# Optimization experiments

Measured on AMD Instinct MI355X. Metric: run time of the kernel, lower is better.

The kernel has to match this reference:

```python
import jax, jax.numpy as jnp
import numpy as np

N_OBJS = 100          # max detections / scatter buffer size
TOP_K = 100           # top_k_n peaks per channel
KP_THRES = 0.3        # score threshold before NMS
NMS_IOU = 0.5
RESIZE_H, RESIZE_W = 1536.0, 1536.0   # resize_shape (== heatmap HxW here)
H, W = 1536, 1536


def _peak_hms(hms):
    # 3x3 stride-1 SAME max pool; keep only local maxima (Base.apply_max_pool)
    hmax = jax.lax.reduce_window(hms, -jnp.inf, jax.lax.max, (1, 3, 3, 1), (1, 1, 1, 1), 'SAME')
    return jnp.where(hms == hmax, hms, 0.0)


def _top_k_loc(hms, k):
    # per-channel top-k peak coordinates -> [b, c, k, 2] (y, x) int32
    b, h, w, c = hms.shape
    flat = jnp.transpose(hms, (0, 3, 1, 2)).reshape(b, c, h * w)
    _, idx = jax.lax.top_k(flat, k)
    return jnp.stack([idx // w, idx % w], axis=-1).astype(jnp.int32)


def _iou_matrix(boxes):
    # boxes [N,4] = (y1,x1,y2,x2)
    y1, x1, y2, x2 = boxes[:, 0], boxes[:, 1], boxes[:, 2], boxes[:, 3]
    area = jnp.maximum(y2 - y1, 0.0) * jnp.maximum(x2 - x1, 0.0)
    iy1 = jnp.maximum(y1[:, None], y1[None, :]); ix1 = jnp.maximum(x1[:, None], x1[None, :])
    iy2 = jnp.minimum(y2[:, None], y2[None, :]); ix2 = jnp.minimum(x2[:, None], x2[None, :])
    inter = jnp.maximum(iy2 - iy1, 0.0) * jnp.maximum(ix2 - ix1, 0.0)
    union = area[:, None] + area[None, :] - inter
    return inter / jnp.maximum(union, 1e-8)


def _nms_single(boxes, scores):
    # greedy single-class NMS, fixed-size (combined_non_max_suppression equivalent,
    # clip_boxes=False, score_threshold=-inf); padded slots are zeros like TF.
    order = jnp.argsort(-scores)
    boxes, scores = boxes[order], scores[order]
    n = boxes.shape[0]
    iou = _iou_matrix(boxes)
    idxs = jnp.arange(n)

    def step(suppressed, inp):
        i, iou_row = inp
        keep_i = ~suppressed[i]
        return suppressed | (keep_i & (iou_row > NMS_IOU) & (idxs > i)), keep_i

    _, keep = jax.lax.scan(step, jnp.zeros(n, bool), (idxs, iou))
    perm = jnp.argsort(jnp.where(keep, 0, 1))  # stable: compact kept to front, score order preserved
    keep_s = keep[perm]
    out_boxes = jnp.where(keep_s[:, None], boxes[perm], 0.0)
    out_scores = jnp.where(keep_s, scores[perm], 0.0)
    return out_boxes, out_scores, jnp.zeros(n, jnp.float32)


def _forward(obj_heat_map, offset_map, size_maps, origin_shapes):
    resize_shape = jnp.array([RESIZE_H, RESIZE_W], jnp.float32)
    ratio = origin_shapes / resize_shape                      # [b,2]
    hms = _peak_hms(obj_heat_map)                             # [b,H,W,2]
    b = hms.shape[0]
    coors = _top_k_loc(hms, TOP_K)                            # [b,2,K,2]
    b_coors, b_lnmks = coors[:, :1], coors[:, 1:]             # obj / nose coords
    bidx = jnp.arange(b)[:, None, None]

    # nose landmark: scores at nose-channel peaks, masked mean of coords (int mean like TF)
    nose_scores = hms[bidx, b_lnmks[..., 0], b_lnmks[..., 1], 1]     # [b,1,K]
    nose_mask = nose_scores > 0.5
    cnt = jnp.maximum(jnp.sum(nose_mask), 1)
    lnmk_mean = jnp.sum(jnp.where(nose_mask[..., None], b_lnmks, 0), axis=(0, 1, 2)) // cnt
    b_lnmks_m = lnmk_mean.reshape(b, 1, 2)                    # requires b == 1 (as in original)
    b_nose_scores = jnp.where(nose_mask, nose_scores, -1.0).reshape(b, -1)

    # boxes from sizes at object peaks
    size_vals = size_maps[bidx, b_coors[..., 0], b_coors[..., 1]]    # [b,1,K,2]
    obj_scores = hms[bidx, b_coors[..., 0], b_coors[..., 1], 0]      # [b,1,K]
    centers = b_coors.astype(jnp.float32)
    tls = jnp.maximum(centers - size_vals / 2.0, 0.0)
    brs = jnp.minimum(centers + size_vals / 2.0, resize_shape - 1.0)
    bboxes = jnp.concatenate([tls, brs], axis=-1) * jnp.tile(ratio, (1, 2))[:, None, None, :]
    bboxes, scores = bboxes[:, 0], obj_scores[:, 0]           # [b,K,4], [b,K]

    # scatter masked candidates into -1-initialized buffer (tensor_scatter_nd_update equivalent)
    mask = scores > KP_THRES
    cand = jnp.where(mask[..., None], jnp.concatenate([bboxes, scores[..., None]], -1), -1.0)
    cand = jnp.pad(cand, ((0, 0), (0, N_OBJS - TOP_K), (0, 0)), constant_values=-1.0)  # [b,N_OBJS,5]

    nb, ns, nc = jax.vmap(_nms_single)(cand[..., :4], cand[..., 4])
    box_results = jnp.where(nb == -1.0, jnp.inf, nb)
    box_results = jnp.where(box_results == 0.0, jnp.inf, box_results)  # (x - 1 == -1)
    b_bboxes = jnp.concatenate([box_results, ns[..., None], nc[..., None]], axis=-1)  # [b,N_OBJS,6]

    # offset vectors at the mean nose landmark (gather 8ch -> [b,n,4,2])
    bidx2 = jnp.arange(b)[:, None]
    off = offset_map[bidx2, b_lnmks_m[..., 0], b_lnmks_m[..., 1]].reshape(b, 1, 4, 2)
    lf = b_lnmks_m.astype(jnp.float32)
    b_ENM = (lf[:, :, None, :] - off) * ratio[:, None, None, :]
    b_lnmks_out = lf * ratio[:, None, :]
    return b_bboxes, b_lnmks_out, b_ENM, b_nose_scores


def setup_inputs() -> dict:
    key = jax.random.key(0)
    k1, k2, k3 = jax.random.split(key, 3)
    obj_heat_map = jax.random.uniform(k1, (1, H, W, 2), jnp.float32)
    offset_map = jax.random.normal(k2, (1, H, W, 8), jnp.float32) * 8.0
    size_maps = jax.random.uniform(k3, (1, H, W, 2), jnp.float32) * 128.0
    origin_shapes = jnp.array([[1080.0, 1920.0]], jnp.float32)
    return {"obj_heat_map": obj_heat_map, "offset_map": offset_map,
            "size_maps": size_maps, "origin_shapes": origin_shapes}


def reference(obj_heat_map, offset_map, size_maps, origin_shapes):
    return _forward(obj_heat_map, offset_map, size_maps, origin_shapes)
```

## Files before the change

### kernel.cpp

```cpp
#include <hip/hip_runtime.h>
#include <cstdint>

#define IW 1536
#define IH 1536
#define TOPK 100
#define CAPP 327680
#define CAPB 128
#define CAPT 8192
#define BF_INF16 0x7F7Fu

typedef unsigned u32; typedef unsigned long long u64; typedef unsigned short u16;

#define OH1   0
#define OCNT  4096
#define OSEL  4102
#define OLSD  4106
#define OZEND 4172
#define OPK   4172
#define OPV   (OPK + 2*CAPP)
#define OLB   (OPV + CAPP)
#define OLT   (OLB + 4*CAPB)

__device__ __forceinline__ u32 enc16(u32 b){ b &= 0xFFFFu; return (b & 0x8000u) ? ((~b)&0xFFFFu) : (b|0x8000u); }
__device__ __forceinline__ u32 dec16(u32 e){ return (e & 0x8000u) ? (e^0x8000u) : ((~e)&0xFFFFu); }
__device__ __forceinline__ float up16(u32 b){ return __uint_as_float((b&0xFFFFu)<<16); }
__device__ __forceinline__ u16 f2bf(float f){ u32 u=__float_as_uint(f); return (u16)((u + 0x7FFFu + ((u>>16)&1u))>>16); }

__device__ __forceinline__ void wave_sel2048(const u32* bins, u32 need, int* Dout, u32* Aout){
  int lane = threadIdx.x & 63;
  u32 s = 0;
  #pragma unroll
  for(int k=0;k<32;++k) s += bins[lane*32+k];
  u32 c = s;
  #pragma unroll
  for(int off=1;off<64;off<<=1){
    u32 v = __shfl_down(c, off, 64);
    if(lane + off < 64) c += v;
  }
  u32 cnext = __shfl_down(c, 1, 64); if(lane==63) cnext = 0u;
  u64 m = __ballot(c >= need);
  if(m == 0ull){ if(lane==0){ *Dout = 0; *Aout = 0u; } return; }
  int L = 63 - __builtin_clzll((unsigned long long)m);
  if(lane == L){
    u32 above = cnext; int D = 32*L;
    for(int b=32*L+31; b>=32*L; --b){
      u32 h = bins[b];
      if(above + h >= need){ D = b; break; }
      above += h;
    }
    *Dout = D; *Aout = above;
  }
}

__global__ __launch_bounds__(1024) void scan_kernel(const u32* __restrict__ hm, u32* __restrict__ ws){
  __shared__ u32 lh[4096];
  __shared__ u32 lbuf[2][1600];
  __shared__ u16 vbuf[2][1600];
  __shared__ u32 lcnt[2], lbase[2];
  int tid = threadIdx.x, lane = tid & 63;
  for(int i=tid;i<4096;i+=1024) lh[i]=0u;
  if(tid<2) lcnt[tid]=0u;
  __syncthreads();

  int p = (blockIdx.x*1024 + tid)*4;
  int y = p / IW, x = p - y*IW;
  const u32* R1 = hm + y*IW;
  const u32* R0 = y ? R1 - IW : R1;
  const u32* R2 = (y < IH-1) ? R1 + IW : R1;
  uint4 c0 = *(const uint4*)(R0+x), c1 = *(const uint4*)(R1+x), c2 = *(const uint4*)(R2+x);
  int xl = x ? x-1 : 0, xr = (x+4 < IW) ? x+4 : IW-1;
  u32 a0[6] = {R0[xl], c0.x, c0.y, c0.z, c0.w, R0[xr]};
  u32 a1[6] = {R1[xl], c1.x, c1.y, c1.z, c1.w, R1[xr]};
  u32 a2[6] = {R2[xl], c2.x, c2.y, c2.z, c2.w, R2[xr]};

  #pragma unroll
  for(int j=0;j<4;++j){
    u32 cc = a1[j+1];
    u32 cl = cc & 0xFFFFu, chv = cc >> 16;
    u32 m0=0u, m1=0u;
    #pragma unroll
    for(int d=0;d<3;++d){
      u32 n0=a0[j+d], n2=a2[j+d]; u32 t;
      t=n0&0xFFFFu; m0=t>m0?t:m0;  t=n0>>16; m1=t>m1?t:m1;
      t=n2&0xFFFFu; m0=t>m0?t:m0;  t=n2>>16; m1=t>m1?t:m1;
    }
    { u32 n=a1[j];   u32 t=n&0xFFFFu; m0=t>m0?t:m0; t=n>>16; m1=t>m1?t:m1; }
    { u32 n=a1[j+2]; u32 t=n&0xFFFFu; m0=t>m0?t:m0; t=n>>16; m1=t>m1?t:m1; }
    bool pk0 = (cl >= m0), pk1 = (chv >= m1);
    u32 idx = (u32)(p + j);

    u64 mk0 = __ballot(pk0);
    if(mk0){
      u32 cw = __popcll(mk0), b;
      if(lane==0) b = atomicAdd(&lcnt[0], cw);
      b = __shfl(b, 0);
      if(pk0){
        u32 pos = b + __popcll(mk0 & ((1ull<<lane)-1ull));
        if(pos < 1600){ lbuf[0][pos] = idx; vbuf[0][pos] = (u16)cl; }
      }
    }
    u64 mk1 = __ballot(pk1);
    if(mk1){
      u32 cw = __popcll(mk1), b;
      if(lane==0) b = atomicAdd(&lcnt[1], cw);
      b = __shfl(b, 0);
      if(pk1){
        u32 pos = b + __popcll(mk1 & ((1ull<<lane)-1ull));
        if(pos < 1600){ lbuf[1][pos] = idx; vbuf[1][pos] = (u16)chv; }
      }
    }
    if(pk0) atomicAdd(&lh[enc16(cl)>>5], 1u);
    if(pk1) atomicAdd(&lh[2048 + (enc16(chv)>>5)], 1u);
  }
  __syncthreads();
  if(tid < 2){
    u32 n = lcnt[tid]; if(n > 1600) n = 1600;
    lcnt[tid] = n;
    lbase[tid] = atomicAdd(&ws[OCNT+tid], n);
  }
  __syncthreads();
  u16* pv = (u16*)(ws + OPV);
  for(int ch=0;ch<2;++ch){
    u32 n = lcnt[ch], base = lbase[ch];
    for(u32 i=tid;i<n;i+=1024){
      u32 g = base + i;
      if(g < CAPP){ ws[OPK + ch*CAPP + g] = lbuf[ch][i]; pv[ch*CAPP + g] = vbuf[ch][i]; }
    }
  }
  for(int i=tid;i<4096;i+=1024) if(lh[i]) atomicAdd(&ws[OH1+i], lh[i]);
}

#define GRID2 128
__global__ __launch_bounds__(1024) void mid_kernel(u32* __restrict__ ws){
  __shared__ u32 lhh[4096];
  __shared__ u64 tbuf[2][2048];
  __shared__ u32 tcnt[2], tbase[2];
  __shared__ u32 lsdl[64];
  __shared__ int Dsh[2]; __shared__ u32 Ash[2];
  int tid = threadIdx.x, lane = tid & 63;
  for(int i=tid;i<4096;i+=1024) lhh[i] = ws[OH1+i];
  if(tid < 2) tcnt[tid] = 0u;
  if(tid < 64) lsdl[tid] = 0u;
  __syncthreads();
  if(tid < 64)       wave_sel2048(lhh,        (u32)TOPK, &Dsh[0], &Ash[0]);
  else if(tid < 128) wave_sel2048(lhh + 2048, (u32)TOPK, &Dsh[1], &Ash[1]);
  __syncthreads();
  if(blockIdx.x == 0 && tid < 2){ ws[OSEL+tid] = (u32)Dsh[tid]; ws[OSEL+2+tid] = Ash[tid]; }

  const u16* pv = (const u16*)(ws + OPV);
  u64* listB = (u64*)(ws + OLB);
  for(int ch=0;ch<2;++ch){
    u32 n = ws[OCNT+ch]; if(n > CAPP) n = CAPP;
    int D = Dsh[ch];
    for(u32 base = blockIdx.x*1024; base < n; base += GRID2*1024){
      u32 i = base + tid;
      bool act = (i < n);
      u32 e = 0, idx = 0;
      if(act){ e = enc16(pv[ch*CAPP + i]); idx = ws[OPK + ch*CAPP + i]; }
      if(act && (int)(e>>5) > D){
        u32 pos = atomicAdd(&ws[OCNT+2+ch], 1u);
        if(pos < CAPB) listB[ch*CAPB + pos] = ((u64)e<<32) | (u32)(~idx);
      }
      bool isT = act && ((int)(e>>5) == D);
      if(isT) atomicAdd(&lsdl[ch*32 + (e & 31u)], 1u);
      u64 mk = __ballot(isT);
      if(mk){
        u32 cw = __popcll(mk), b;
        if(lane==0) b = atomicAdd(&tcnt[ch], cw);
        b = __shfl(b, 0);
        if(isT){
          u32 pos = b + __popcll(mk & ((1ull<<lane)-1ull));
          if(pos < 2048) tbuf[ch][pos] = ((u64)e<<32) | (u32)(~idx);
        }
      }
    }
  }
  __syncthreads();
  if(tid < 2){
    u32 c = tcnt[tid]; if(c > 2048) c = 2048;
    tcnt[tid] = c;
    tbase[tid] = atomicAdd(&ws[OCNT+4+tid], c);
  }
  __syncthreads();
  u64* tie = (u64*)(ws + OLT);
  for(int ch=0;ch<2;++ch)
    for(u32 i=tid;i<tcnt[ch];i+=1024){
      u32 g = tbase[ch] + i;
      if(g < CAPT) tie[ch*CAPT + g] = tbuf[ch][i];
    }
  if(tid < 64 && lsdl[tid]) atomicAdd(&ws[OLSD + tid], lsdl[tid]);
}

__global__ __launch_bounds__(512) void finalize_kernel(
    u32* __restrict__ ws, const u32* __restrict__ szm, const u16* __restrict__ offm,
    const u16* __restrict__ orig, u16* __restrict__ out){
  __shared__ u32 tidxS[2][CAPT];
  __shared__ u32 h2s[2][2048];
  __shared__ u64 keysS[2][CAPB];
  __shared__ u32 selS[2][CAPB];
  __shared__ u32 wbitsS[2][64];
  __shared__ u32 lsdS[64];
  __shared__ u32 hdr[10];
  __shared__ int selcS[2], selc2S[2], BvS[2], LshS[2], tcS[2];
  __shared__ float oval[TOPK]; __shared__ int oidx[TOPK];
  __shared__ float nval[TOPK]; __shared__ int nidx[TOPK];
  __shared__ float cbox[TOPK][4]; __shared__ float cscore[TOPK]; __shared__ float area[TOPK];
  __shared__ int sup[TOPK]; __shared__ int slotv[TOPK];
  __shared__ u64 nbits[2*TOPK];
  __shared__ u64 suppS[2];
  __shared__ int cS, srS, scS, meanr, meanc;
  int tid = threadIdx.x, lane = tid & 63;
  int ch = tid >> 8, ltid = tid & 255;

  if(tid < 10) hdr[tid] = ws[OCNT + tid];
  if(tid < 64) lsdS[tid] = ws[OLSD + tid];
  for(int i=tid;i<4096;i+=512) ((u32*)h2s)[i] = 0u;
  if(tid < 128) ((u32*)wbitsS)[tid] = 0u;
  if(tid < 4){ selcS[tid&1] = 0; selc2S[tid&1] = 0; }
  if(tid < 2){ BvS[tid] = 0; LshS[tid] = 0; tcS[tid] = 0; }
  if(tid < TOPK){ oval[tid]=0.0f; oidx[tid]=0; nval[tid]=0.0f; nidx[tid]=0; }
  __syncthreads();

  int nB = (int)hdr[2+ch]; if(nB > CAPB) nB = CAPB;
  int nT = (int)hdr[4+ch]; if(nT > CAPT) nT = CAPT;
  int D  = (int)hdr[6+ch];
  u32 above = hdr[8+ch];
  const u64* listB = ((const u64*)(ws + OLB)) + ch*CAPB;
  const u64* tie   = ((const u64*)(ws + OLT)) + ch*CAPT;
  float* dval = ch ? nval : oval;
  int*   didx = ch ? nidx : oidx;

  if(ltid < 64){
    u32 h = (lane < 32) ? lsdS[ch*32 + lane] : 0u;
    u32 c = h;
    #pragma unroll
    for(int off=1;off<32;off<<=1){
      u32 v = __shfl_down(c, off, 64);
      if(lane + off < 32) c += v;
    }
    u32 need2 = (u32)TOPK - above;
    u64 m = __ballot(lane >= 1 && lane < 32 && c >= need2);
    if(lane == 0){
      LshS[ch] = m ? (63 - __builtin_clzll((unsigned long long)m)) : 0;
      selcS[ch] = nB;
    }
  }
  for(int i=ltid;i<nB;i+=256) keysS[ch][i] = listB[i];
  __syncthreads();
  u32 thr = ((u32)D<<5) | (u32)LshS[ch];
  float tval = up16(dec16(thr));

  for(int base2=0; base2<nT; base2+=256){
    int i = base2 + ltid;
    bool act = (i < nT);
    u64 k = 0; u32 e = 0, idx = 0;
    if(act){ k = tie[i]; e = (u32)(k>>32); idx = ~(u32)(k & 0xFFFFFFFFu); }
    if(act && e > thr){
      int pos = atomicAdd(&selcS[ch], 1); if(pos < CAPB) keysS[ch][pos] = k;
    }
    bool isT = act && (e == thr);
    u64 mk = __ballot(isT);
    if(mk){
      u32 cw = __popcll(mk), b;
      if(lane==0) b = (u32)atomicAdd(&tcS[ch], (int)cw);
      b = __shfl(b, 0);
      if(isT){
        u32 pos = b + __popcll(mk & ((1ull<<lane)-1ull));
        if(pos < CAPT) tidxS[ch][pos] = idx;
      }
    }
    if(isT) atomicAdd(&h2s[ch][idx>>11], 1u);
  }
  __syncthreads();

  int nA = selcS[ch]; if(nA > CAPB) nA = CAPB; if(nA > TOPK) nA = TOPK;
  int need = TOPK - nA;
  if(ltid < nA){
    u64 kreg = keysS[ch][ltid];
    int r = 0;
    for(int j=0;j<nA;++j) r += (keysS[ch][j] > kreg);
    if(r < TOPK){
      dval[r] = up16(dec16((u32)(kreg>>32)));
      didx[r] = (int)(~(u32)(kreg & 0xFFFFFFFFu));
    }
  }
  if(ltid < 64){
    const u32* hh = h2s[ch];
    int base = lane*32;
    u32 s = 0;
    #pragma unroll
    for(int k2=0;k2<32;++k2) s += hh[base+k2];
    u32 c = s;
    #pragma unroll
    for(int off=1;off<64;off<<=1){
      u32 v = __shfl_up(c, off, 64);
      if(lane >= off) c += v;
    }
    u64 m = __ballot(need > 0 && c >= (u32)need);
    int L = m ? (int)(__ffsll((unsigned long long)m) - 1) : -1;
    if(L >= 0 && lane == L){
      u32 hb[32];
      #pragma unroll
      for(int k2=0;k2<32;++k2) hb[k2] = hh[base+k2];
      u32 cum2 = c - s;
      int Bsel = base;
      #pragma unroll
      for(int k2=0;k2<32;++k2){
        if(cum2 + hb[k2] >= (u32)need){ Bsel = base+k2; break; }
        cum2 += hb[k2];
      }
      BvS[ch] = Bsel;
    }
  }
  __syncthreads();

  int B = BvS[ch];
  int tc = tcS[ch]; if(tc > CAPT) tc = CAPT;
  if(need > 0){
    for(int i=ltid;i<tc;i+=256){
      u32 idx = tidxS[ch][i];
      int b = (int)(idx>>11);
      if(b < B){
        int pos = atomicAdd(&selc2S[ch], 1);
        if(pos < CAPB) selS[ch][pos] = idx;
      } else if(b == B){
        atomicOr(&wbitsS[ch][(idx&2047)>>5], 1u<<(idx&31));
      }
    }
  }
  __syncthreads();

  int sc = selc2S[ch]; if(sc > CAPB) sc = CAPB;
  if(need > 0 && ltid < sc){
    u32 v = selS[ch][ltid];
    int r = 0;
    for(int j=0;j<sc;++j) r += (selS[ch][j] < v);
    if(nA + r < TOPK){ dval[nA+r] = tval; didx[nA+r] = (int)v; }
  }
  if(need > 0 && ltid < 64){
    u32 bits = wbitsS[ch][ltid];
    u32 cnt = __popc(bits);
    u32 incl = cnt;
    #pragma unroll
    for(int off=1;off<64;off<<=1){
      u32 v = __shfl_up(incl, off, 64);
      if(lane >= off) incl += v;
    }
    int excl = (int)(incl - cnt);
    int rem = need - sc;
    int pos = nA + sc + excl;
    int j = 0;
    while(bits){
      int l = __ffs(bits) - 1; bits &= bits - 1;
      if(excl + j < rem && pos + j < TOPK){
        dval[pos+j] = tval;
        didx[pos+j] = (int)(((u32)B<<11) | ((u32)ltid<<5) | (u32)l);
      }
      ++j;
    }
  }
  __syncthreads();

  float ry = up16(orig[0]) / 1536.0f;
  float rx = up16(orig[1]) / 1536.0f;

  if(tid == 0){ cS = 0; srS = 0; scS = 0; }
  __syncthreads();
  if(tid < TOPK && nval[tid] > 0.5f){
    atomicAdd(&cS, 1);
    atomicAdd(&srS, nidx[tid] / IW);
    atomicAdd(&scS, nidx[tid] % IW);
  }
  if(tid < TOPK) out[610 + tid] = f2bf(nval[tid] > 0.5f ? nval[tid] : -1.0f);
  __syncthreads();
  if(tid == 0){
    int c = cS < 1 ? 1 : cS;
    meanr = srS / c; meanc = scS / c;
  }

  if(tid < TOPK){
    int idx = oidx[tid];
    int r = idx / IW, c = idx - r*IW;
    float score = oval[tid];
    u32 sz = szm[idx];
    float sy = up16(sz), sx = up16(sz>>16);
    float cy = (float)r, cx = (float)c;
    float tly = fmaxf(cy - sy*0.5f, 0.0f);
    float tlx = fmaxf(cx - sx*0.5f, 0.0f);
    float bry = fminf(cy + sy*0.5f, 1535.0f);
    float brx = fminf(cx + sx*0.5f, 1535.0f);
    bool mk = score > 0.3f;
    float b0 = mk ? tly*ry : -1.0f;
    float b1 = mk ? tlx*rx : -1.0f;
    float b2 = mk ? bry*ry : -1.0f;
    float b3 = mk ? brx*rx : -1.0f;
    cbox[tid][0]=b0; cbox[tid][1]=b1; cbox[tid][2]=b2; cbox[tid][3]=b3;
    cscore[tid] = mk ? score : -1.0f;
    area[tid] = fmaxf(b2-b0,0.0f) * fmaxf(b3-b1,0.0f);
  }
  if(tid < 2*TOPK) nbits[tid] = 0ull;
  __syncthreads();

  for(int t=tid; t<TOPK*TOPK; t+=512){
    int i = t / TOPK, j = t - i*TOPK;
    if(j > i){
      float iy1 = fmaxf(cbox[i][0], cbox[j][0]);
      float ix1 = fmaxf(cbox[i][1], cbox[j][1]);
      float iy2 = fminf(cbox[i][2], cbox[j][2]);
      float ix2 = fminf(cbox[i][3], cbox[j][3]);
      float inter = fmaxf(iy2-iy1,0.0f) * fmaxf(ix2-ix1,0.0f);
      float uni = (area[i] + area[j]) - inter;
      if(inter / fmaxf(uni, 1e-8f) > 0.5f)
        atomicOr(&nbits[i*2 + (j>>6)], 1ull << (j&63));
    }
  }
  __syncthreads();
  if(tid == 0){
    u64 s0 = 0ull, s1 = 0ull;
    for(int base=0;base<TOPK;base+=10){
      u64 buf[20];
      #pragma unroll
      for(int k=0;k<20;++k) buf[k] = nbits[2*base+k];
      #pragma unroll
      for(int k=0;k<10;++k){
        int i = base+k;
        bool su = (i<64) ? ((s0>>i)&1ull) : ((s1>>(i-64))&1ull);
        if(!su){ s0 |= buf[2*k]; s1 |= buf[2*k+1]; }
      }
    }
    suppS[0] = s0; suppS[1] = s1;
  }
  __syncthreads();
  if(tid < TOPK) sup[tid] = (int)((suppS[tid>>6] >> (tid&63)) & 1ull);
  __syncthreads();

  if(tid < TOPK){
    int kbefore = 0, sbefore = 0, ktot = 0;
    for(int j=0;j<TOPK;++j){
      int sj = sup[j];
      ktot += (1 - sj);
      if(j < tid){ kbefore += (1 - sj); sbefore += sj; }
    }
    int slot = sup[tid] ? (ktot + sbefore) : kbefore;
    slotv[slot] = tid;
  }
  __syncthreads();

  if(tid < TOPK){
    int s = slotv[tid];
    bool ks = !sup[s];
    u16 row[6];
    if(ks){
      for(int d=0;d<4;++d){
        float v = cbox[s][d];
        row[d] = (v == -1.0f || v == 0.0f) ? (u16)BF_INF16 : f2bf(v);
      }
      row[4] = f2bf(cscore[s]);
    } else {
      for(int d=0;d<4;++d) row[d] = (u16)BF_INF16;
      row[4] = 0;
    }
    row[5] = 0;
    for(int d=0;d<6;++d) out[tid*6 + d] = row[d];
  }

  if(tid == 0){
    float lfy = (float)meanr, lfx = (float)meanc;
    out[600] = f2bf(lfy * ry);
    out[601] = f2bf(lfx * rx);
    const u16* op = offm + ((size_t)meanr*IW + meanc)*8;
    for(int p=0;p<4;++p){
      out[602 + p*2 + 0] = f2bf((lfy - up16(op[p*2+0])) * ry);
      out[602 + p*2 + 1] = f2bf((lfx - up16(op[p*2+1])) * rx);
    }
  }
}

extern "C" void kernel_launch(void* const* d_in, const int* in_sizes, int n_in,
                              void* d_out, int out_size, void* d_ws, size_t ws_size,
                              hipStream_t stream) {
  const u32* heat = (const u32*)d_in[0];
  const u16* offm = (const u16*)d_in[1];
  const u32* szm  = (const u32*)d_in[2];
  const u16* orig = (const u16*)d_in[3];
  u16* out = (u16*)d_out;
  u32* ws = (u32*)d_ws;

  hipMemsetAsync(ws, 0, OZEND*sizeof(u32), stream);
  scan_kernel<<<576, 1024, 0, stream>>>(heat, ws);
  mid_kernel<<<GRID2, 1024, 0, stream>>>(ws);
  finalize_kernel<<<1, 512, 0, stream>>>(ws, szm, offm, orig, out);
}
```

Baseline: 183.2 us.

## Fuse scan, mid and finalize kernels into one persistent kernel with grid barriers

Result: slower. 197.3 us (+7.7%).

```diff
diff --git a/kernel.cpp b/kernel.cpp
--- a/kernel.cpp
+++ b/kernel.cpp
@@ -9,12 +9,16 @@
 #define CAPT 8192
 #define BF_INF16 0x7F7Fu
 
+#define NBLK 192
+#define VBTOT 576
+
 typedef unsigned u32; typedef unsigned long long u64; typedef unsigned short u16;
 
 #define OH1   0
 #define OCNT  4096
 #define OSEL  4102
 #define OLSD  4106
+#define OBAR  4170
 #define OZEND 4172
 #define OPK   4172
 #define OPV   (OPK + 2*CAPP)
@@ -52,125 +56,166 @@
   }
 }
 
-__global__ __launch_bounds__(1024) void scan_kernel(const u32* __restrict__ hm, u32* __restrict__ ws){
-  __shared__ u32 lh[4096];
-  __shared__ u32 lbuf[2][1600];
-  __shared__ u16 vbuf[2][1600];
-  __shared__ u32 lcnt[2], lbase[2];
+union SMem {
+  struct {
+    u32 lh[4096];
+    u32 lbuf[2][1600];
+    u16 vbuf[2][1600];
+  } a;
+  struct {
+    u32 lhh[4096];
+    u64 tbuf[2][2048];
+    u32 lsdl[64];
+  } b;
+  struct {
+    u32 tidxS[2][CAPT];
+    u32 h2s[2][2048];
+    u64 keysS[2][CAPB];
+    u32 selS[2][CAPB];
+    u32 wbitsS[2][64];
+    u32 lsdS[64];
+    u32 hdr[10];
+    float oval[TOPK]; int oidx[TOPK];
+    float nval[TOPK]; int nidx[TOPK];
+    float cbox[TOPK][4]; float cscore[TOPK]; float area[TOPK];
+    int sup[TOPK]; int slotv[TOPK];
+    u64 nbits[2*TOPK];
+  } c;
+};
+
+__global__ __launch_bounds__(1024, 4) void fused_kernel(
+    const u32* __restrict__ hm, u32* __restrict__ ws,
+    const u32* __restrict__ szm, const u16* __restrict__ offm,
+    const u16* __restrict__ orig, u16* __restrict__ out){
+  __shared__ SMem S;
+  __shared__ u32 lcnt[2], lbase[2], tcnt[2], tbase[2];
+  __shared__ int Dsh[2]; __shared__ u32 Ash[2];
+  __shared__ int selcS[2], selc2S[2], BvS[2], LshS[2], tcS[2];
+  __shared__ u64 suppS[2];
+  __shared__ int cS, srS, scS, meanr, meanc;
+
   int tid = threadIdx.x, lane = tid & 63;
-  for(int i=tid;i<4096;i+=1024) lh[i]=0u;
-  if(tid<2) lcnt[tid]=0u;
-  __syncthreads();
-
-  int p = (blockIdx.x*1024 + tid)*4;
-  int y = p / IW, x = p - y*IW;
-  const u32* R1 = hm + y*IW;
-  const u32* R0 = y ? R1 - IW : R1;
-  const u32* R2 = (y < IH-1) ? R1 + IW : R1;
-  uint4 c0 = *(const uint4*)(R0+x), c1 = *(const uint4*)(R1+x), c2 = *(const uint4*)(R2+x);
-  int xl = x ? x-1 : 0, xr = (x+4 < IW) ? x+4 : IW-1;
-  u32 a0[6] = {R0[xl], c0.x, c0.y, c0.z, c0.w, R0[xr]};
-  u32 a1[6] = {R1[xl], c1.x, c1.y, c1.z, c1.w, R1[xr]};
-  u32 a2[6] = {R2[xl], c2.x, c2.y, c2.z, c2.w, R2[xr]};
-
-  #pragma unroll
-  for(int j=0;j<4;++j){
-    u32 cc = a1[j+1];
-    u32 cl = cc & 0xFFFFu, chv = cc >> 16;
-    u32 m0=0u, m1=0u;
+
+  for(int i=tid;i<4096;i+=1024) S.a.lh[i]=0u;
+  for(int vb = blockIdx.x; vb < VBTOT; vb += NBLK){
+    __syncthreads();
+    if(tid<2) lcnt[tid]=0u;
+    __syncthreads();
+
+    int p = (vb*1024 + tid)*4;
+    int y = p / IW, x = p - y*IW;
+    const u32* R1 = hm + y*IW;
+    const u32* R0 = y ? R1 - IW : R1;
+    const u32* R2 = (y < IH-1) ? R1 + IW : R1;
+    uint4 c0 = *(const uint4*)(R0+x), c1 = *(const uint4*)(R1+x), c2 = *(const uint4*)(R2+x);
+    int xl = x ? x-1 : 0, xr = (x+4 < IW) ? x+4 : IW-1;
+    u32 a0[6] = {R0[xl], c0.x, c0.y, c0.z, c0.w, R0[xr]};
+    u32 a1[6] = {R1[xl], c1.x, c1.y, c1.z, c1.w, R1[xr]};
+    u32 a2[6] = {R2[xl], c2.x, c2.y, c2.z, c2.w, R2[xr]};
+
     #pragma unroll
-    for(int d=0;d<3;++d){
-      u32 n0=a0[j+d], n2=a2[j+d]; u32 t;
-      t=n0&0xFFFFu; m0=t>m0?t:m0;  t=n0>>16; m1=t>m1?t:m1;
-      t=n2&0xFFFFu; m0=t>m0?t:m0;  t=n2>>16; m1=t>m1?t:m1;
-    }
-    { u32 n=a1[j];   u32 t=n&0xFFFFu; m0=t>m0?t:m0; t=n>>16; m1=t>m1?t:m1; }
-    { u32 n=a1[j+2]; u32 t=n&0xFFFFu; m0=t>m0?t:m0; t=n>>16; m1=t>m1?t:m1; }
-    bool pk0 = (cl >= m0), pk1 = (chv >= m1);
-    u32 idx = (u32)(p + j);
-
-    u64 mk0 = __ballot(pk0);
-    if(mk0){
-      u32 cw = __popcll(mk0), b;
-      if(lane==0) b = atomicAdd(&lcnt[0], cw);
-      b = __shfl(b, 0);
-      if(pk0){
-        u32 pos = b + __popcll(mk0 & ((1ull<<lane)-1ull));
-        if(pos < 1600){ lbuf[0][pos] = idx; vbuf[0][pos] = (u16)cl; }
-      }
-    }
-    u64 mk1 = __ballot(pk1);
-    if(mk1){
-      u32 cw = __popcll(mk1), b;
-      if(lane==0) b = atomicAdd(&lcnt[1], cw);
-      b = __shfl(b, 0);
-      if(pk1){
-        u32 pos = b + __popcll(mk1 & ((1ull<<lane)-1ull));
-        if(pos < 1600){ lbuf[1][pos] = idx; vbuf[1][pos] = (u16)chv; }
-      }
-    }
-    if(pk0) atomicAdd(&lh[enc16(cl)>>5], 1u);
-    if(pk1) atomicAdd(&lh[2048 + (enc16(chv)>>5)], 1u);
-  }
-  __syncthreads();
-  if(tid < 2){
-    u32 n = lcnt[tid]; if(n > 1600) n = 1600;
-    lcnt[tid] = n;
-    lbase[tid] = atomicAdd(&ws[OCNT+tid], n);
-  }
-  __syncthreads();
-  u16* pv = (u16*)(ws + OPV);
-  for(int ch=0;ch<2;++ch){
-    u32 n = lcnt[ch], base = lbase[ch];
-    for(u32 i=tid;i<n;i+=1024){
-      u32 g = base + i;
-      if(g < CAPP){ ws[OPK + ch*CAPP + g] = lbuf[ch][i]; pv[ch*CAPP + g] = vbuf[ch][i]; }
-    }
-  }
-  for(int i=tid;i<4096;i+=1024) if(lh[i]) atomicAdd(&ws[OH1+i], lh[i]);
-}
-
-#define GRID2 128
-__global__ __launch_bounds__(1024) void mid_kernel(u32* __restrict__ ws){
-  __shared__ u32 lhh[4096];
-  __shared__ u64 tbuf[2][2048];
-  __shared__ u32 tcnt[2], tbase[2];
-  __shared__ u32 lsdl[64];
-  __shared__ int Dsh[2]; __shared__ u32 Ash[2];
-  int tid = threadIdx.x, lane = tid & 63;
-  for(int i=tid;i<4096;i+=1024) lhh[i] = ws[OH1+i];
+    for(int j=0;j<4;++j){
+      u32 cc = a1[j+1];
+      u32 cl = cc & 0xFFFFu, chv = cc >> 16;
+      u32 m0=0u, m1=0u;
+      #pragma unroll
+      for(int d=0;d<3;++d){
+        u32 n0=a0[j+d], n2=a2[j+d]; u32 t;
+        t=n0&0xFFFFu; m0=t>m0?t:m0;  t=n0>>16; m1=t>m1?t:m1;
+        t=n2&0xFFFFu; m0=t>m0?t:m0;  t=n2>>16; m1=t>m1?t:m1;
+      }
+      { u32 n=a1[j];   u32 t=n&0xFFFFu; m0=t>m0?t:m0; t=n>>16; m1=t>m1?t:m1; }
+      { u32 n=a1[j+2]; u32 t=n&0xFFFFu; m0=t>m0?t:m0; t=n>>16; m1=t>m1?t:m1; }
+      bool pk0 = (cl >= m0), pk1 = (chv >= m1);
+      u32 idx = (u32)(p + j);
+
+      u64 mk0 = __ballot(pk0);
+      if(mk0){
+        u32 cw = __popcll(mk0), b;
+        if(lane==0) b = atomicAdd(&lcnt[0], cw);
+        b = __shfl(b, 0);
+        if(pk0){
+          u32 pos = b + __popcll(mk0 & ((1ull<<lane)-1ull));
+          if(pos < 1600){ S.a.lbuf[0][pos] = idx; S.a.vbuf[0][pos] = (u16)cl; }
+        }
+      }
+      u64 mk1 = __ballot(pk1);
+      if(mk1){
+        u32 cw = __popcll(mk1), b;
+        if(lane==0) b = atomicAdd(&lcnt[1], cw);
+        b = __shfl(b, 0);
+        if(pk1){
+          u32 pos = b + __popcll(mk1 & ((1ull<<lane)-1ull));
+          if(pos < 1600){ S.a.lbuf[1][pos] = idx; S.a.vbuf[1][pos] = (u16)chv; }
+        }
+      }
+      if(pk0) atomicAdd(&S.a.lh[enc16(cl)>>5], 1u);
+      if(pk1) atomicAdd(&S.a.lh[2048 + (enc16(chv)>>5)], 1u);
+    }
+    __syncthreads();
+    if(tid < 2){
+      u32 n = lcnt[tid]; if(n > 1600) n = 1600;
+      lcnt[tid] = n;
+      lbase[tid] = atomicAdd(&ws[OCNT+tid], n);
+    }
+    __syncthreads();
+    {
+      u16* pvw = (u16*)(ws + OPV);
+      for(int ch2=0;ch2<2;++ch2){
+        u32 n = lcnt[ch2], base = lbase[ch2];
+        for(u32 i=tid;i<n;i+=1024){
+          u32 g = base + i;
+          if(g < CAPP){ ws[OPK + ch2*CAPP + g] = S.a.lbuf[ch2][i]; pvw[ch2*CAPP + g] = S.a.vbuf[ch2][i]; }
+        }
+      }
+    }
+  }
+  __syncthreads();
+  for(int i=tid;i<4096;i+=1024) if(S.a.lh[i]) atomicAdd(&ws[OH1+i], S.a.lh[i]);
+
+  __syncthreads();
+  if(tid==0){
+    __hip_atomic_fetch_add(&ws[OBAR], 1u, __ATOMIC_RELEASE, __HIP_MEMORY_SCOPE_AGENT);
+    while(__hip_atomic_load(&ws[OBAR], __ATOMIC_ACQUIRE, __HIP_MEMORY_SCOPE_AGENT) < (u32)NBLK)
+      __builtin_amdgcn_s_sleep(2);
+  }
+  __syncthreads();
+
+  for(int i=tid;i<4096;i+=1024) S.b.lhh[i] = ws[OH1+i];
   if(tid < 2) tcnt[tid] = 0u;
-  if(tid < 64) lsdl[tid] = 0u;
-  __syncthreads();
-  if(tid < 64)       wave_sel2048(lhh,        (u32)TOPK, &Dsh[0], &Ash[0]);
-  else if(tid < 128) wave_sel2048(lhh + 2048, (u32)TOPK, &Dsh[1], &Ash[1]);
+  if(tid < 64) S.b.lsdl[tid] = 0u;
+  __syncthreads();
+  if(tid < 64)       wave_sel2048(S.b.lhh,        (u32)TOPK, &Dsh[0], &Ash[0]);
+  else if(tid < 128) wave_sel2048(S.b.lhh + 2048, (u32)TOPK, &Dsh[1], &Ash[1]);
   __syncthreads();
   if(blockIdx.x == 0 && tid < 2){ ws[OSEL+tid] = (u32)Dsh[tid]; ws[OSEL+2+tid] = Ash[tid]; }
 
-  const u16* pv = (const u16*)(ws + OPV);
-  u64* listB = (u64*)(ws + OLB);
-  for(int ch=0;ch<2;++ch){
-    u32 n = ws[OCNT+ch]; if(n > CAPP) n = CAPP;
-    int D = Dsh[ch];
-    for(u32 base = blockIdx.x*1024; base < n; base += GRID2*1024){
-      u32 i = base + tid;
-      bool act = (i < n);
-      u32 e = 0, idx = 0;
-      if(act){ e = enc16(pv[ch*CAPP + i]); idx = ws[OPK + ch*CAPP + i]; }
-      if(act && (int)(e>>5) > D){
-        u32 pos = atomicAdd(&ws[OCNT+2+ch], 1u);
-        if(pos < CAPB) listB[ch*CAPB + pos] = ((u64)e<<32) | (u32)(~idx);
-      }
-      bool isT = act && ((int)(e>>5) == D);
-      if(isT) atomicAdd(&lsdl[ch*32 + (e & 31u)], 1u);
-      u64 mk = __ballot(isT);
-      if(mk){
-        u32 cw = __popcll(mk), b;
-        if(lane==0) b = atomicAdd(&tcnt[ch], cw);
-        b = __shfl(b, 0);
-        if(isT){
-          u32 pos = b + __popcll(mk & ((1ull<<lane)-1ull));
-          if(pos < 2048) tbuf[ch][pos] = ((u64)e<<32) | (u32)(~idx);
+  {
+    const u16* pvr = (const u16*)(ws + OPV);
+    u64* listBw = (u64*)(ws + OLB);
+    for(int ch2=0;ch2<2;++ch2){
+      u32 n = ws[OCNT+ch2]; if(n > CAPP) n = CAPP;
+      int D2 = Dsh[ch2];
+      for(u32 base = blockIdx.x*1024; base < n; base += (u32)NBLK*1024){
+        u32 i = base + tid;
+        bool act = (i < n);
+        u32 e = 0, idx = 0;
+        if(act){ e = enc16(pvr[ch2*CAPP + i]); idx = ws[OPK + ch2*CAPP + i]; }
+        if(act && (int)(e>>5) > D2){
+          u32 pos = atomicAdd(&ws[OCNT+2+ch2], 1u);
+          if(pos < CAPB) listBw[ch2*CAPB + pos] = ((u64)e<<32) | (u32)(~idx);
+        }
+        bool isT = act && ((int)(e>>5) == D2);
+        if(isT) atomicAdd(&S.b.lsdl[ch2*32 + (e & 31u)], 1u);
+        u64 mk = __ballot(isT);
+        if(mk){
+          u32 cw = __popcll(mk), b;
+          if(lane==0) b = atomicAdd(&tcnt[ch2], cw);
+          b = __shfl(b, 0);
+          if(isT){
+            u32 pos = b + __popcll(mk & ((1ull<<lane)-1ull));
+            if(pos < 2048) S.b.tbuf[ch2][pos] = ((u64)e<<32) | (u32)(~idx);
+          }
         }
       }
     }
@@ -182,296 +227,306 @@
     tbase[tid] = atomicAdd(&ws[OCNT+4+tid], c);
   }
   __syncthreads();
-  u64* tie = (u64*)(ws + OLT);
-  for(int ch=0;ch<2;++ch)
-    for(u32 i=tid;i<tcnt[ch];i+=1024){
-      u32 g = tbase[ch] + i;
-      if(g < CAPT) tie[ch*CAPT + g] = tbuf[ch][i];
-    }
-  if(tid < 64 && lsdl[tid]) atomicAdd(&ws[OLSD + tid], lsdl[tid]);
-}
-
-__global__ __launch_bounds__(512) void finalize_kernel(
-    u32* __restrict__ ws, const u32* __restrict__ szm, const u16* __restrict__ offm,
-    const u16* __restrict__ orig, u16* __restrict__ out){
-  __shared__ u32 tidxS[2][CAPT];
-  __shared__ u32 h2s[2][2048];
-  __shared__ u64 keysS[2][CAPB];
-  __shared__ u32 selS[2][CAPB];
-  __shared__ u32 wbitsS[2][64];
-  __shared__ u32 lsdS[64];
-  __shared__ u32 hdr[10];
-  __shared__ int selcS[2], selc2S[2], BvS[2], LshS[2], tcS[2];
-  __shared__ float oval[TOPK]; __shared__ int oidx[TOPK];
-  __shared__ float nval[TOPK]; __shared__ int nidx[TOPK];
-  __shared__ float cbox[TOPK][4]; __shared__ float cscore[TOPK]; __shared__ float area[TOPK];
-  __shared__ int sup[TOPK]; __shared__ int slotv[TOPK];
-  __shared__ u64 nbits[2*TOPK];
-  __shared__ u64 suppS[2];
-  __shared__ int cS, srS, scS, meanr, meanc;
-  int tid = threadIdx.x, lane = tid & 63;
-  int ch = tid >> 8, ltid = tid & 255;
-
-  if(tid < 10) hdr[tid] = ws[OCNT + tid];
-  if(tid < 64) lsdS[tid] = ws[OLSD + tid];
-  for(int i=tid;i<4096;i+=512) ((u32*)h2s)[i] = 0u;
-  if(tid < 128) ((u32*)wbitsS)[tid] = 0u;
-  if(tid < 4){ selcS[tid&1] = 0; selc2S[tid&1] = 0; }
-  if(tid < 2){ BvS[tid] = 0; LshS[tid] = 0; tcS[tid] = 0; }
-  if(tid < TOPK){ oval[tid]=0.0f; oidx[tid]=0; nval[tid]=0.0f; nidx[tid]=0; }
-  __syncthreads();
-
-  int nB = (int)hdr[2+ch]; if(nB > CAPB) nB = CAPB;
-  int nT = (int)hdr[4+ch]; if(nT > CAPT) nT = CAPT;
-  int D  = (int)hdr[6+ch];
-  u32 above = hdr[8+ch];
-  const u64* listB = ((const u64*)(ws + OLB)) + ch*CAPB;
-  const u64* tie   = ((const u64*)(ws + OLT)) + ch*CAPT;
-  float* dval = ch ? nval : oval;
-  int*   didx = ch ? nidx : oidx;
-
-  if(ltid < 64){
-    u32 h = (lane < 32) ? lsdS[ch*32 + lane] : 0u;
-    u32 c = h;
-    #pragma unroll
-    for(int off=1;off<32;off<<=1){
-      u32 v = __shfl_down(c, off, 64);
-      if(lane + off < 32) c += v;
-    }
-    u32 need2 = (u32)TOPK - above;
-    u64 m = __ballot(lane >= 1 && lane < 32 && c >= need2);
-    if(lane == 0){
-      LshS[ch] = m ? (63 - __builtin_clzll((unsigned long long)m)) : 0;
-      selcS[ch] = nB;
-    }
-  }
-  for(int i=ltid;i<nB;i+=256) keysS[ch][i] = listB[i];
-  __syncthreads();
-  u32 thr = ((u32)D<<5) | (u32)LshS[ch];
-  float tval = up16(dec16(thr));
-
-  for(int base2=0; base2<nT; base2+=256){
-    int i = base2 + ltid;
-    bool act = (i < nT);
-    u64 k = 0; u32 e = 0, idx = 0;
-    if(act){ k = tie[i]; e = (u32)(k>>32); idx = ~(u32)(k & 0xFFFFFFFFu); }
-    if(act && e > thr){
-      int pos = atomicAdd(&selcS[ch], 1); if(pos < CAPB) keysS[ch][pos] = k;
-    }
-    bool isT = act && (e == thr);
-    u64 mk = __ballot(isT);
-    if(mk){
-      u32 cw = __popcll(mk), b;
-      if(lane==0) b = (u32)atomicAdd(&tcS[ch], (int)cw);
-      b = __shfl(b, 0);
-      if(isT){
-        u32 pos = b + __popcll(mk & ((1ull<<lane)-1ull));
-        if(pos < CAPT) tidxS[ch][pos] = idx;
-      }
-    }
-    if(isT) atomicAdd(&h2s[ch][idx>>11], 1u);
-  }
-  __syncthreads();
-
-  int nA = selcS[ch]; if(nA > CAPB) nA = CAPB; if(nA > TOPK) nA = TOPK;
-  int need = TOPK - nA;
-  if(ltid < nA){
-    u64 kreg = keysS[ch][ltid];
-    int r = 0;
-    for(int j=0;j<nA;++j) r += (keysS[ch][j] > kreg);
-    if(r < TOPK){
-      dval[r] = up16(dec16((u32)(kreg>>32)));
-      didx[r] = (int)(~(u32)(kreg & 0xFFFFFFFFu));
-    }
-  }
-  if(ltid < 64){
-    const u32* hh = h2s[ch];
-    int base = lane*32;
-    u32 s = 0;
-    #pragma unroll
-    for(int k2=0;k2<32;++k2) s += hh[base+k2];
-    u32 c = s;
-    #pragma unroll
-    for(int off=1;off<64;off<<=1){
-      u32 v = __shfl_up(c, off, 64);
-      if(lane >= off) c += v;
-    }
-    u64 m = __ballot(need > 0 && c >= (u32)need);
-    int L = m ? (int)(__ffsll((unsigned long long)m) - 1) : -1;
-    if(L >= 0 && lane == L){
-      u32 hb[32];
+  {
+    u64* tieW = (u64*)(ws + OLT);
+    for(int ch2=0;ch2<2;++ch2)
+      for(u32 i=tid;i<tcnt[ch2];i+=1024){
+        u32 g = tbase[ch2] + i;
+        if(g < CAPT) tieW[ch2*CAPT + g] = S.b.tbuf[ch2][i];
+      }
+  }
+  if(tid < 64 && S.b.lsdl[tid]) atomicAdd(&ws[OLSD + tid], S.b.lsdl[tid]);
+
+  __syncthreads();
+  if(blockIdx.x != 0){
+    if(tid==0) __hip_atomic_fetch_add(&ws[OBAR+1], 1u, __ATOMIC_RELEASE, __HIP_MEMORY_SCOPE_AGENT);
+    return;
+  }
+  if(tid==0){
+    __hip_atomic_fetch_add(&ws[OBAR+1], 1u, __ATOMIC_RELEASE, __HIP_MEMORY_SCOPE_AGENT);
+    while(__hip_atomic_load(&ws[OBAR+1], __ATOMIC_ACQUIRE, __HIP_MEMORY_SCOPE_AGENT) < (u32)NBLK)
+      __builtin_amdgcn_s_sleep(2);
+  }
+  __syncthreads();
+
+  {
+    bool act5 = (tid < 512);
+    int ch = (tid >> 8) & 1, ltid = tid & 255;
+
+    if(tid < 10) S.c.hdr[tid] = ws[OCNT + tid];
+    if(tid < 64) S.c.lsdS[tid] = ws[OLSD + tid];
+    for(int i=tid;i<4096;i+=1024) ((u32*)S.c.h2s)[i] = 0u;
+    if(tid < 128) ((u32*)S.c.wbitsS)[tid] = 0u;
+    if(tid < 4){ selcS[tid&1] = 0; selc2S[tid&1] = 0; }
+    if(tid < 2){ BvS[tid] = 0; LshS[tid] = 0; tcS[tid] = 0; }
+    if(tid < TOPK){ S.c.oval[tid]=0.0f; S.c.oidx[tid]=0; S.c.nval[tid]=0.0f; S.c.nidx[tid]=0; }
+    __syncthreads();
+
+    int nB=0, nT=0, D=0; u32 above=0;
+    const u64* listB = nullptr; const u64* tie = nullptr;
+    float* dval = nullptr; int* didx = nullptr;
+    if(act5){
+      nB = (int)S.c.hdr[2+ch]; if(nB > CAPB) nB = CAPB;
+      nT = (int)S.c.hdr[4+ch]; if(nT > CAPT) nT = CAPT;
+      D  = (int)S.c.hdr[6+ch];
+      above = S.c.hdr[8+ch];
+      listB = ((const u64*)(ws + OLB)) + ch*CAPB;
+      tie   = ((const u64*)(ws + OLT)) + ch*CAPT;
+      dval = ch ? S.c.nval : S.c.oval;
+      didx = ch ? S.c.nidx : S.c.oidx;
+    }
+
+    if(act5 && ltid < 64){
+      u32 h = (lane < 32) ? S.c.lsdS[ch*32 + lane] : 0u;
+      u32 c = h;
       #pragma unroll
-      for(int k2=0;k2<32;++k2) hb[k2] = hh[base+k2];
-      u32 cum2 = c - s;
-      int Bsel = base;
-      #pragma unroll
-      for(int k2=0;k2<32;++k2){
-        if(cum2 + hb[k2] >= (u32)need){ Bsel = base+k2; break; }
-        cum2 += hb[k2];
-      }
-      BvS[ch] = Bsel;
-    }
-  }
-  __syncthreads();
-
-  int B = BvS[ch];
-  int tc = tcS[ch]; if(tc > CAPT) tc = CAPT;
-  if(need > 0){
-    for(int i=ltid;i<tc;i+=256){
-      u32 idx = tidxS[ch][i];
-      int b = (int)(idx>>11);
-      if(b < B){
-        int pos = atomicAdd(&selc2S[ch], 1);
-        if(pos < CAPB) selS[ch][pos] = idx;
-      } else if(b == B){
-        atomicOr(&wbitsS[ch][(idx&2047)>>5], 1u<<(idx&31));
-      }
-    }
-  }
-  __syncthreads();
-
-  int sc = selc2S[ch]; if(sc > CAPB) sc = CAPB;
-  if(need > 0 && ltid < sc){
-    u32 v = selS[ch][ltid];
-    int r = 0;
-    for(int j=0;j<sc;++j) r += (selS[ch][j] < v);
-    if(nA + r < TOPK){ dval[nA+r] = tval; didx[nA+r] = (int)v; }
-  }
-  if(need > 0 && ltid < 64){
-    u32 bits = wbitsS[ch][ltid];
-    u32 cnt = __popc(bits);
-    u32 incl = cnt;
-    #pragma unroll
-    for(int off=1;off<64;off<<=1){
-      u32 v = __shfl_up(incl, off, 64);
-      if(lane >= off) incl += v;
-    }
-    int excl = (int)(incl - cnt);
-    int rem = need - sc;
-    int pos = nA + sc + excl;
-    int j = 0;
-    while(bits){
-      int l = __ffs(bits) - 1; bits &= bits - 1;
-      if(excl + j < rem && pos + j < TOPK){
-        dval[pos+j] = tval;
-        didx[pos+j] = (int)(((u32)B<<11) | ((u32)ltid<<5) | (u32)l);
-      }
-      ++j;
-    }
-  }
-  __syncthreads();
-
-  float ry = up16(orig[0]) / 1536.0f;
-  float rx = up16(orig[1]) / 1536.0f;
-
-  if(tid == 0){ cS = 0; srS = 0; scS = 0; }
-  __syncthreads();
-  if(tid < TOPK && nval[tid] > 0.5f){
-    atomicAdd(&cS, 1);
-    atomicAdd(&srS, nidx[tid] / IW);
-    atomicAdd(&scS, nidx[tid] % IW);
-  }
-  if(tid < TOPK) out[610 + tid] = f2bf(nval[tid] > 0.5f ? nval[tid] : -1.0f);
-  __syncthreads();
-  if(tid == 0){
-    int c = cS < 1 ? 1 : cS;
-    meanr = srS / c; meanc = scS / c;
-  }
-
-  if(tid < TOPK){
-    int idx = oidx[tid];
-    int r = idx / IW, c = idx - r*IW;
-    float score = oval[tid];
-    u32 sz = szm[idx];
-    float sy = up16(sz), sx = up16(sz>>16);
-    float cy = (float)r, cx = (float)c;
-    float tly = fmaxf(cy - sy*0.5f, 0.0f);
-    float tlx = fmaxf(cx - sx*0.5f, 0.0f);
-    float bry = fminf(cy + sy*0.5f, 1535.0f);
-    float brx = fminf(cx + sx*0.5f, 1535.0f);
-    bool mk = score > 0.3f;
-    float b0 = mk ? tly*ry : -1.0f;
-    float b1 = mk ? tlx*rx : -1.0f;
-    float b2 = mk ? bry*ry : -1.0f;
-    float b3 = mk ? brx*rx : -1.0f;
-    cbox[tid][0]=b0; cbox[tid][1]=b1; cbox[tid][2]=b2; cbox[tid][3]=b3;
-    cscore[tid] = mk ? score : -1.0f;
-    area[tid] = fmaxf(b2-b0,0.0f) * fmaxf(b3-b1,0.0f);
-  }
-  if(tid < 2*TOPK) nbits[tid] = 0ull;
-  __syncthreads();
-
-  for(int t=tid; t<TOPK*TOPK; t+=512){
-    int i = t / TOPK, j = t - i*TOPK;
-    if(j > i){
-      float iy1 = fmaxf(cbox[i][0], cbox[j][0]);
-      float ix1 = fmaxf(cbox[i][1], cbox[j][1]);
-      float iy2 = fminf(cbox[i][2], cbox[j][2]);
-      float ix2 = fminf(cbox[i][3], cbox[j][3]);
-      float inter = fmaxf(iy2-iy1,0.0f) * fmaxf(ix2-ix1,0.0f);
-      float uni = (area[i] + area[j]) - inter;
-      if(inter / fmaxf(uni, 1e-8f) > 0.5f)
-        atomicOr(&nbits[i*2 + (j>>6)], 1ull << (j&63));
-    }
-  }
-  __syncthreads();
-  if(tid == 0){
-    u64 s0 = 0ull, s1 = 0ull;
-    for(int base=0;base<TOPK;base+=10){
-      u64 buf[20];
-      #pragma unroll
-      for(int k=0;k<20;++k) buf[k] = nbits[2*base+k];
-      #pragma unroll
-      for(int k=0;k<10;++k){
-        int i = base+k;
-        bool su = (i<64) ? ((s0>>i)&1ull) : ((s1>>(i-64))&1ull);
-        if(!su){ s0 |= buf[2*k]; s1 |= buf[2*k+1]; }
-      }
-    }
-    suppS[0] = s0; suppS[1] = s1;
-  }
-  __syncthreads();
-  if(tid < TOPK) sup[tid] = (int)((suppS[tid>>6] >> (tid&63)) & 1ull);
-  __syncthreads();
-
-  if(tid < TOPK){
-    int kbefore = 0, sbefore = 0, ktot = 0;
-    for(int j=0;j<TOPK;++j){
-      int sj = sup[j];
-      ktot += (1 - sj);
-      if(j < tid){ kbefore += (1 - sj); sbefore += sj; }
-    }
-    int slot = sup[tid] ? (ktot + sbefore) : kbefore;
-    slotv[slot] = tid;
-  }
-  __syncthreads();
-
-  if(tid < TOPK){
-    int s = slotv[tid];
-    bool ks = !sup[s];
-    u16 row[6];
-    if(ks){
-      for(int d=0;d<4;++d){
-        float v = cbox[s][d];
-        row[d] = (v == -1.0f || v == 0.0f) ? (u16)BF_INF16 : f2bf(v);
-      }
-      row[4] = f2bf(cscore[s]);
-    } else {
-      for(int d=0;d<4;++d) row[d] = (u16)BF_INF16;
-      row[4] = 0;
-    }
-    row[5] = 0;
-    for(int d=0;d<6;++d) out[tid*6 + d] = row[d];
-  }
-
-  if(tid == 0){
-    float lfy = (float)meanr, lfx = (float)meanc;
-    out[600] = f2bf(lfy * ry);
-    out[601] = f2bf(lfx * rx);
-    const u16* op = offm + ((size_t)meanr*IW + meanc)*8;
-    for(int p=0;p<4;++p){
-      out[602 + p*2 + 0] = f2bf((lfy - up16(op[p*2+0])) * ry);
-      out[602 + p*2 + 1] = f2bf((lfx - up16(op[p*2+1])) * rx);
+      for(int off=1;off<32;off<<=1){
+        u32 v = __shfl_down(c, off, 64);
+        if(lane + off < 32) c += v;
+      }
+      u32 need2 = (u32)TOPK - above;
+      u64 m = __ballot(lane >= 1 && lane < 32 && c >= need2);
+      if(lane == 0){
+        LshS[ch] = m ? (63 - __builtin_clzll((unsigned long long)m)) : 0;
+        selcS[ch] = nB;
+      }
+    }
+    if(act5) for(int i=ltid;i<nB;i+=256) S.c.keysS[ch][i] = listB[i];
+    __syncthreads();
+    u32 thr = 0; float tval = 0.0f;
+    if(act5){ thr = ((u32)D<<5) | (u32)LshS[ch]; tval = up16(dec16(thr)); }
+
+    if(act5) for(int base2=0; base2<nT; base2+=256){
+      int i = base2 + ltid;
+      bool act = (i < nT);
+      u64 k = 0; u32 e = 0, idx = 0;
+      if(act){ k = tie[i]; e = (u32)(k>>32); idx = ~(u32)(k & 0xFFFFFFFFu); }
+      if(act && e > thr){
+        int pos = atomicAdd(&selcS[ch], 1); if(pos < CAPB) S.c.keysS[ch][pos] = k;
+      }
+      bool isT = act && (e == thr);
+      u64 mk = __ballot(isT);
+      if(mk){
+        u32 cw = __popcll(mk), b;
+        if(lane==0) b = (u32)atomicAdd(&tcS[ch], (int)cw);
+        b = __shfl(b, 0);
+        if(isT){
+          u32 pos = b + __popcll(mk & ((1ull<<lane)-1ull));
+          if(pos < CAPT) S.c.tidxS[ch][pos] = idx;
+        }
+      }
+      if(isT) atomicAdd(&S.c.h2s[ch][idx>>11], 1u);
+    }
+    __syncthreads();
+
+    int nA = 0, need = 0;
+    if(act5){
+      nA = selcS[ch]; if(nA > CAPB) nA = CAPB; if(nA > TOPK) nA = TOPK;
+      need = TOPK - nA;
+      if(ltid < nA){
+        u64 kreg = S.c.keysS[ch][ltid];
+        int r = 0;
+        for(int j=0;j<nA;++j) r += (S.c.keysS[ch][j] > kreg);
+        if(r < TOPK){
+          dval[r] = up16(dec16((u32)(kreg>>32)));
+          didx[r] = (int)(~(u32)(kreg & 0xFFFFFFFFu));
+        }
+      }
+      if(ltid < 64){
+        const u32* hh = S.c.h2s[ch];
+        int base = lane*32;
+        u32 s = 0;
+        #pragma unroll
+        for(int k2=0;k2<32;++k2) s += hh[base+k2];
+        u32 c = s;
+        #pragma unroll
+        for(int off=1;off<64;off<<=1){
+          u32 v = __shfl_up(c, off, 64);
+          if(lane >= off) c += v;
+        }
+        u64 m = __ballot(need > 0 && c >= (u32)need);
+        int L = m ? (int)(__ffsll((unsigned long long)m) - 1) : -1;
+        if(L >= 0 && lane == L){
+          u32 hb[32];
+          #pragma unroll
+          for(int k2=0;k2<32;++k2) hb[k2] = hh[base+k2];
+          u32 cum2 = c - s;
+          int Bsel = base;
+          #pragma unroll
+          for(int k2=0;k2<32;++k2){
+            if(cum2 + hb[k2] >= (u32)need){ Bsel = base+k2; break; }
+            cum2 += hb[k2];
+          }
+          BvS[ch] = Bsel;
+        }
+      }
+    }
+    __syncthreads();
+
+    int B = 0, tc = 0;
+    if(act5){
+      B = BvS[ch];
+      tc = tcS[ch]; if(tc > CAPT) tc = CAPT;
+      if(need > 0){
+        for(int i=ltid;i<tc;i+=256){
+          u32 idx = S.c.tidxS[ch][i];
+          int b = (int)(idx>>11);
+          if(b < B){
+            int pos = atomicAdd(&selc2S[ch], 1);
+            if(pos < CAPB) S.c.selS[ch][pos] = idx;
+          } else if(b == B){
+            atomicOr(&S.c.wbitsS[ch][(idx&2047)>>5], 1u<<(idx&31));
+          }
+        }
+      }
+    }
+    __syncthreads();
+
+    if(act5){
+      int sc = selc2S[ch]; if(sc > CAPB) sc = CAPB;
+      if(need > 0 && ltid < sc){
+        u32 v = S.c.selS[ch][ltid];
+        int r = 0;
+        for(int j=0;j<sc;++j) r += (S.c.selS[ch][j] < v);
+        if(nA + r < TOPK){ dval[nA+r] = tval; didx[nA+r] = (int)v; }
+      }
+      if(need > 0 && ltid < 64){
+        u32 bits = S.c.wbitsS[ch][ltid];
+        u32 cnt = __popc(bits);
+        u32 incl = cnt;
+        #pragma unroll
+        for(int off=1;off<64;off<<=1){
+          u32 v = __shfl_up(incl, off, 64);
+          if(lane >= off) incl += v;
+        }
+        int excl = (int)(incl - cnt);
+        int rem = need - sc;
+        int pos = nA + sc + excl;
+        int j = 0;
+        while(bits){
+          int l = __ffs(bits) - 1; bits &= bits - 1;
+          if(excl + j < rem && pos + j < TOPK){
+            dval[pos+j] = tval;
+            didx[pos+j] = (int)(((u32)B<<11) | ((u32)ltid<<5) | (u32)l);
+          }
+          ++j;
+        }
+      }
+    }
+    __syncthreads();
+
+    float ry = up16(orig[0]) / 1536.0f;
+    float rx = up16(orig[1]) / 1536.0f;
+
+    if(tid == 0){ cS = 0; srS = 0; scS = 0; }
+    __syncthreads();
+    if(tid < TOPK && S.c.nval[tid] > 0.5f){
+      atomicAdd(&cS, 1);
+      atomicAdd(&srS, S.c.nidx[tid] / IW);
+      atomicAdd(&scS, S.c.nidx[tid] % IW);
+    }
+    if(tid < TOPK) out[610 + tid] = f2bf(S.c.nval[tid] > 0.5f ? S.c.nval[tid] : -1.0f);
+    __syncthreads();
+    if(tid == 0){
+      int c = cS < 1 ? 1 : cS;
+      meanr = srS / c; meanc = scS / c;
+    }
+
+    if(tid < TOPK){
+      int idx = S.c.oidx[tid];
+      int r = idx / IW, c = idx - r*IW;
+      float score = S.c.oval[tid];
+      u32 sz = szm[idx];
+      float sy = up16(sz), sx = up16(sz>>16);
+      float cy = (float)r, cx = (float)c;
+      float tly = fmaxf(cy - sy*0.5f, 0.0f);
+      float tlx = fmaxf(cx - sx*0.5f, 0.0f);
+      float bry = fminf(cy + sy*0.5f, 1535.0f);
+      float brx = fminf(cx + sx*0.5f, 1535.0f);
+      bool mk = score > 0.3f;
+      float b0 = mk ? tly*ry : -1.0f;
+      float b1 = mk ? tlx*rx : -1.0f;
+      float b2 = mk ? bry*ry : -1.0f;
+      float b3 = mk ? brx*rx : -1.0f;
+      S.c.cbox[tid][0]=b0; S.c.cbox[tid][1]=b1; S.c.cbox[tid][2]=b2; S.c.cbox[tid][3]=b3;
+      S.c.cscore[tid] = mk ? score : -1.0f;
+      S.c.area[tid] = fmaxf(b2-b0,0.0f) * fmaxf(b3-b1,0.0f);
+    }
+    if(tid < 2*TOPK) S.c.nbits[tid] = 0ull;
+    __syncthreads();
+
+    for(int t=tid; t<TOPK*TOPK; t+=1024){
+      int i = t / TOPK, j = t - i*TOPK;
+      if(j > i){
+        float iy1 = fmaxf(S.c.cbox[i][0], S.c.cbox[j][0]);
+        float ix1 = fmaxf(S.c.cbox[i][1], S.c.cbox[j][1]);
+        float iy2 = fminf(S.c.cbox[i][2], S.c.cbox[j][2]);
+        float ix2 = fminf(S.c.cbox[i][3], S.c.cbox[j][3]);
+        float inter = fmaxf(iy2-iy1,0.0f) * fmaxf(ix2-ix1,0.0f);
+        float uni = (S.c.area[i] + S.c.area[j]) - inter;
+        if(inter / fmaxf(uni, 1e-8f) > 0.5f)
+          atomicOr(&S.c.nbits[i*2 + (j>>6)], 1ull << (j&63));
+      }
+    }
+    __syncthreads();
+    if(tid == 0){
+      u64 s0 = 0ull, s1 = 0ull;
+      for(int base=0;base<TOPK;base+=10){
+        u64 buf[20];
+        #pragma unroll
+        for(int k=0;k<20;++k) buf[k] = S.c.nbits[2*base+k];
+        #pragma unroll
+        for(int k=0;k<10;++k){
+          int i = base+k;
+          bool su = (i<64) ? ((s0>>i)&1ull) : ((s1>>(i-64))&1ull);
+          if(!su){ s0 |= buf[2*k]; s1 |= buf[2*k+1]; }
+        }
+      }
+      suppS[0] = s0; suppS[1] = s1;
+    }
+    __syncthreads();
+    if(tid < TOPK) S.c.sup[tid] = (int)((suppS[tid>>6] >> (tid&63)) & 1ull);
+    __syncthreads();
+
+    if(tid < TOPK){
+      int kbefore = 0, sbefore = 0, ktot = 0;
+      for(int j=0;j<TOPK;++j){
+        int sj = S.c.sup[j];
+        ktot += (1 - sj);
+        if(j < tid){ kbefore += (1 - sj); sbefore += sj; }
+      }
+      int slot = S.c.sup[tid] ? (ktot + sbefore) : kbefore;
+      S.c.slotv[slot] = tid;
+    }
+    __syncthreads();
+
+    if(tid < TOPK){
+      int s = S.c.slotv[tid];
+      bool ks = !S.c.sup[s];
+      u16 row[6];
+      if(ks){
+        for(int d=0;d<4;++d){
+          float v = S.c.cbox[s][d];
+          row[d] = (v == -1.0f || v == 0.0f) ? (u16)BF_INF16 : f2bf(v);
+        }
+        row[4] = f2bf(S.c.cscore[s]);
+      } else {
+        for(int d=0;d<4;++d) row[d] = (u16)BF_INF16;
+        row[4] = 0;
+      }
+      row[5] = 0;
+      for(int d=0;d<6;++d) out[tid*6 + d] = row[d];
+    }
+
+    if(tid == 0){
+      float lfy = (float)meanr, lfx = (float)meanc;
+      out[600] = f2bf(lfy * ry);
+      out[601] = f2bf(lfx * rx);
+      const u16* op = offm + ((size_t)meanr*IW + meanc)*8;
+      for(int p=0;p<4;++p){
+        out[602 + p*2 + 0] = f2bf((lfy - up16(op[p*2+0])) * ry);
+        out[602 + p*2 + 1] = f2bf((lfx - up16(op[p*2+1])) * rx);
+      }
     }
   }
 }
@@ -487,7 +542,5 @@
   u32* ws = (u32*)d_ws;
 
   hipMemsetAsync(ws, 0, OZEND*sizeof(u32), stream);
-  scan_kernel<<<576, 1024, 0, stream>>>(heat, ws);
-  mid_kernel<<<GRID2, 1024, 0, stream>>>(ws);
-  finalize_kernel<<<1, 512, 0, stream>>>(ws, szm, offm, orig, out);
+  fused_kernel<<<NBLK, 1024, 0, stream>>>(heat, ws, szm, offm, orig, out);
 }
```
